# Kernel tuning notes

Hardware: AMD Instinct MI355X
Metric: run time of the kernel (lower is better)

The kernel has to match this reference:

```python
import jax, jax.numpy as jnp
import numpy as np

TEMPERATURE = 8.0  # sqrt(d_k=64)
NEG_FILL = -1000.0


def setup_inputs() -> dict:
    key = jax.random.key(0)
    k1, k2, k3, k4 = jax.random.split(key, 4)
    B, Lq, Lk, D = 16, 2048, 2048, 64
    q = jax.random.normal(k1, (B, Lq, D), dtype=jnp.float32)
    k = jax.random.normal(k2, (B, Lk, D), dtype=jnp.float32)
    v = jax.random.normal(k3, (B, Lk, D), dtype=jnp.float32)
    pad_mask = jax.random.randint(k4, (B, Lk), 0, 2).astype(bool)
    return {"q": q, "k": k, "v": v, "pad_mask": pad_mask}


def reference(q, k, v, pad_mask):
    # scores: [B, Lq, Lk]
    attn = jnp.einsum('bqd,bkd->bqk', q, k) / TEMPERATURE
    # mask padded keys (broadcast over query dim, like pad_mask.unsqueeze(1))
    attn = jnp.where(pad_mask[:, None, :], NEG_FILL, attn)
    attn = jax.nn.softmax(attn, axis=-1)
    # dropout is identity in eval / p=0
    output = jnp.einsum('bqk,bkd->bqd', attn, v)
    return output, attn
```

## Files before the change

kernel.cpp:

```cpp
#include <hip/hip_runtime.h>
#include <hip/hip_bf16.h>

#define BB 16
#define LL 2048
#define DD 64

typedef __attribute__((ext_vector_type(8))) short short8t;
typedef __attribute__((ext_vector_type(4))) float f32x4;
typedef __attribute__((ext_vector_type(4))) unsigned short ushort4t;

__device__ __forceinline__ unsigned short f2bf(float x) {
  union { float f; unsigned int u; } c; c.f = x;
  unsigned int u = c.u;
  u += 0x7fffu + ((u >> 16) & 1u);
  return (unsigned short)(u >> 16);
}

__global__ void cvt_bf16(const float* __restrict__ in, unsigned short* __restrict__ out) {
  int i = (blockIdx.x * 256 + threadIdx.x) * 4;
  float4 v = *(const float4*)(in + i);
  ushort4t o;
  o.x = f2bf(v.x); o.y = f2bf(v.y); o.z = f2bf(v.z); o.w = f2bf(v.w);
  *(ushort4t*)(out + i) = o;
}

__global__ void vtrans(const float* __restrict__ v, unsigned short* __restrict__ vt) {
  __shared__ unsigned short t[64][66];
  int b = blockIdx.x >> 5, j0 = (blockIdx.x & 31) * 64;
  const float* src = v + ((size_t)b * LL + j0) * DD;
#pragma unroll
  for (int i = 0; i < 16; ++i) {
    int lin = i * 256 + threadIdx.x;
    int j = lin >> 6, d = lin & 63;
    t[j][d] = f2bf(src[lin]);
  }
  __syncthreads();
  unsigned short* dst = vt + (size_t)b * DD * LL;
#pragma unroll
  for (int i = 0; i < 16; ++i) {
    int lin = i * 256 + threadIdx.x;
    int d = lin >> 6, j = lin & 63;
    dst[(size_t)d * LL + j0 + j] = t[j][d];
  }
}

__device__ __forceinline__ void async_cp16(const unsigned short* src, unsigned short* dst_lds) {
  __builtin_amdgcn_global_load_lds(
      (const __attribute__((address_space(1))) unsigned int*)src,
      (__attribute__((address_space(3))) unsigned int*)dst_lds, 16, 0, 0);
}

__global__ void __launch_bounds__(256, 2)
attn_main(const unsigned short* __restrict__ Qb, const unsigned short* __restrict__ Kb,
          const unsigned short* __restrict__ VTb, const int* __restrict__ mask,
          float* __restrict__ out, float* __restrict__ attn) {
  __shared__ __align__(16) unsigned short TB[4][3][2048];
  __shared__ float redL[4][64];
  __shared__ float rinvL[64];

  const int tid = threadIdx.x;
  const int w = tid >> 6;
  const int l = tid & 63;
  const int l15 = l & 15;
  const int g = l >> 4;

  const int b = blockIdx.x >> 5;
  const int q0 = (blockIdx.x & 31) << 6;

  unsigned short* KB = &TB[w][0][0];
  unsigned short* VB = &TB[w][1][0];
  unsigned short* PB = &TB[w][2][0];

  const unsigned short* Kbb = Kb + (size_t)b * LL * DD;
  const unsigned short* VTbb = VTb + (size_t)b * DD * LL;
  const int* maskb = mask + b * LL;

  short8t qf[4][2];
  {
    const unsigned short* qbase = Qb + ((size_t)b * LL + q0 + l15) * DD + 8 * g;
#pragma unroll
    for (int mi = 0; mi < 4; ++mi)
#pragma unroll
      for (int h = 0; h < 2; ++h)
        qf[mi][h] = *(const short8t*)(qbase + mi * 16 * DD + 32 * h);
  }

  float ls[4][4];
#pragma unroll
  for (int mi = 0; mi < 4; ++mi)
#pragma unroll
    for (int r = 0; r < 4; ++r) ls[mi][r] = 0.f;

  for (int t = w; t < 64; t += 4) {
    const int k0 = t * 32;
    {
      const unsigned short* gs = Kbb + (size_t)k0 * DD;
#pragma unroll
      for (int i = 0; i < 4; ++i) {
        int row = i * 8 + (l >> 3);
        int ce = (l & 7) * 8;
        async_cp16(gs + row * 64 + (ce ^ ((row & 3) << 4)), KB + i * 512);
      }
    }
    int mk0 = maskb[k0 + l15];
    int mk1 = maskb[k0 + 16 + l15];
    asm volatile("s_waitcnt vmcnt(0)" ::: "memory");

    f32x4 sacc[4][2] = {};
    short8t kf[2][2];
#pragma unroll
    for (int ni = 0; ni < 2; ++ni)
#pragma unroll
      for (int h = 0; h < 2; ++h) {
        int row = 16 * ni + l15;
        int col = (32 * h + 8 * g) ^ ((l15 & 3) << 4);
        kf[ni][h] = *(const short8t*)(KB + row * 64 + col);
      }
#pragma unroll
    for (int mi = 0; mi < 4; ++mi)
#pragma unroll
      for (int ni = 0; ni < 2; ++ni)
#pragma unroll
        for (int h = 0; h < 2; ++h)
          sacc[mi][ni] = __builtin_amdgcn_mfma_f32_16x16x32_bf16(qf[mi][h], kf[ni][h], sacc[mi][ni], 0, 0, 0);

#pragma unroll
    for (int mi = 0; mi < 4; ++mi)
#pragma unroll
      for (int ni = 0; ni < 2; ++ni) {
        int mk = ni ? mk1 : mk0;
#pragma unroll
        for (int r = 0; r < 4; ++r) {
          float sv = mk ? -1000.f : sacc[mi][ni][r] * 0.125f;
          ls[mi][r] += __expf(sv);
        }
      }
  }

#pragma unroll
  for (int mi = 0; mi < 4; ++mi)
#pragma unroll
    for (int r = 0; r < 4; ++r) {
      float s = ls[mi][r];
      s += __shfl_xor(s, 1);
      s += __shfl_xor(s, 2);
      s += __shfl_xor(s, 4);
      s += __shfl_xor(s, 8);
      if (l15 == 0) redL[w][16 * mi + 4 * g + r] = s;
    }
  __syncthreads();
  if (tid < 64)
    rinvL[tid] = 1.0f / (redL[0][tid] + redL[1][tid] + redL[2][tid] + redL[3][tid]);
  __syncthreads();

  float rinv_[4][4];
#pragma unroll
  for (int mi = 0; mi < 4; ++mi)
#pragma unroll
    for (int r = 0; r < 4; ++r) rinv_[mi][r] = rinvL[16 * mi + 4 * g + r];

  f32x4 oacc[4][4] = {};
  for (int t = w; t < 64; t += 4) {
    const int k0 = t * 32;
    {
      const unsigned short* gs = Kbb + (size_t)k0 * DD;
#pragma unroll
      for (int i = 0; i < 4; ++i) {
        int row = i * 8 + (l >> 3);
        int ce = (l & 7) * 8;
        async_cp16(gs + row * 64 + (ce ^ ((row & 3) << 4)), KB + i * 512);
      }
    }
    {
      const unsigned short* gs = VTbb + k0;
#pragma unroll
      for (int i = 0; i < 4; ++i) {
        int row = i * 16 + (l >> 2);
        int ce = (l & 3) * 8;
        async_cp16(gs + (size_t)row * LL + (ce ^ ((row & 1) << 4)), VB + i * 512);
      }
    }
    int mk0 = maskb[k0 + l15];
    int mk1 = maskb[k0 + 16 + l15];
    asm volatile("s_waitcnt vmcnt(0)" ::: "memory");

    f32x4 sacc[4][2] = {};
    short8t kf[2][2];
#pragma unroll
    for (int ni = 0; ni < 2; ++ni)
#pragma unroll
      for (int h = 0; h < 2; ++h) {
        int row = 16 * ni + l15;
        int col = (32 * h + 8 * g) ^ ((l15 & 3) << 4);
        kf[ni][h] = *(const short8t*)(KB + row * 64 + col);
      }
#pragma unroll
    for (int mi = 0; mi < 4; ++mi)
#pragma unroll
      for (int ni = 0; ni < 2; ++ni)
#pragma unroll
        for (int h = 0; h < 2; ++h)
          sacc[mi][ni] = __builtin_amdgcn_mfma_f32_16x16x32_bf16(qf[mi][h], kf[ni][h], sacc[mi][ni], 0, 0, 0);

#pragma unroll
    for (int mi = 0; mi < 4; ++mi)
#pragma unroll
      for (int ni = 0; ni < 2; ++ni) {
        int mk = ni ? mk1 : mk0;
#pragma unroll
        for (int r = 0; r < 4; ++r) {
          float sv = mk ? -1000.f : sacc[mi][ni][r] * 0.125f;
          float p = __expf(sv) * rinv_[mi][r];
          int qloc = 16 * mi + 4 * g + r;
          attn[((size_t)(b * LL + q0 + qloc)) * LL + k0 + 16 * ni + l15] = p;
          PB[qloc * 32 + ((16 * ni + l15) ^ ((r & 1) << 4))] = f2bf(p);
        }
      }

    short8t pf[4], vf[4];
#pragma unroll
    for (int mi = 0; mi < 4; ++mi)
      pf[mi] = *(const short8t*)(PB + (16 * mi + l15) * 32 + ((8 * g) ^ ((l & 1) << 4)));
#pragma unroll
    for (int ni = 0; ni < 4; ++ni)
      vf[ni] = *(const short8t*)(VB + (16 * ni + l15) * 32 + ((8 * g) ^ ((l & 1) << 4)));
#pragma unroll
    for (int mi = 0; mi < 4; ++mi)
#pragma unroll
      for (int ni = 0; ni < 4; ++ni)
        oacc[mi][ni] = __builtin_amdgcn_mfma_f32_16x16x32_bf16(pf[mi], vf[ni], oacc[mi][ni], 0, 0, 0);
  }

  __syncthreads();
  float* OB = (float*)&TB[0][0][0];
  if (w) {
#pragma unroll
    for (int mi = 0; mi < 4; ++mi)
#pragma unroll
      for (int ni = 0; ni < 4; ++ni)
#pragma unroll
        for (int r = 0; r < 4; ++r)
          OB[(w - 1) * 4096 + (16 * mi + 4 * g + r) * 64 + 16 * ni + l15] = oacc[mi][ni][r];
  }
  __syncthreads();
  if (w == 0) {
#pragma unroll
    for (int mi = 0; mi < 4; ++mi)
#pragma unroll
      for (int ni = 0; ni < 4; ++ni)
#pragma unroll
        for (int r = 0; r < 4; ++r) {
          int pos = (16 * mi + 4 * g + r) * 64 + 16 * ni + l15;
          float o = oacc[mi][ni][r] + OB[pos] + OB[4096 + pos] + OB[8192 + pos];
          out[((size_t)(b * LL + q0 + 16 * mi + 4 * g + r)) * DD + 16 * ni + l15] = o;
        }
  }
}

extern "C" void kernel_launch(void* const* d_in, const int* in_sizes, int n_in,
                              void* d_out, int out_size, void* d_ws, size_t ws_size,
                              hipStream_t stream) {
  const float* q = (const float*)d_in[0];
  const float* k = (const float*)d_in[1];
  const float* v = (const float*)d_in[2];
  const int* pm = (const int*)d_in[3];

  float* out = (float*)d_out;
  float* attn = out + (size_t)BB * LL * DD;

  unsigned short* Qb = (unsigned short*)d_ws;
  unsigned short* Kb = Qb + (size_t)BB * LL * DD;
  unsigned short* VT = Kb + (size_t)BB * LL * DD;

  cvt_bf16<<<2048, 256, 0, stream>>>(q, Qb);
  cvt_bf16<<<2048, 256, 0, stream>>>(k, Kb);
  vtrans<<<512, 256, 0, stream>>>(v, VT);
  attn_main<<<512, 256, 0, stream>>>(Qb, Kb, VT, pm, out, attn);
}
```

Baseline: 100.3 us.

## Repartition attention by query rows per wave with shared double-buffered K/V tiles

Merges the three preprocessing kernels into one prep launch. In the main kernel, each wave now owns 16 query rows and loops over all keys, instead of splitting the key range across waves. This removes the cross-wave softmax-sum and output reductions through LDS. K tiles of 128 keys are shared block-wide and double-buffered with async LDS loads; the next tile's K, V and mask are prefetched while MFMAs run. Probabilities are staged in LDS so attn is written with coalesced vector stores. Also adds block-index swizzling, setprio around MFMAs and masked-exp skipping, at the cost of more block barriers and more LDS per block.

New measurement: 103.9 us. 3.7% more time.

```diff
diff --git a/kernel.cpp b/kernel.cpp
--- a/kernel.cpp
+++ b/kernel.cpp
@@ -16,31 +16,38 @@
   return (unsigned short)(u >> 16);
 }
 
-__global__ void cvt_bf16(const float* __restrict__ in, unsigned short* __restrict__ out) {
-  int i = (blockIdx.x * 256 + threadIdx.x) * 4;
-  float4 v = *(const float4*)(in + i);
-  ushort4t o;
-  o.x = f2bf(v.x); o.y = f2bf(v.y); o.z = f2bf(v.z); o.w = f2bf(v.w);
-  *(ushort4t*)(out + i) = o;
-}
-
-__global__ void vtrans(const float* __restrict__ v, unsigned short* __restrict__ vt) {
+__global__ void prep(const float* __restrict__ q, const float* __restrict__ k,
+                     const float* __restrict__ v,
+                     unsigned short* __restrict__ Qb, unsigned short* __restrict__ Kb,
+                     unsigned short* __restrict__ VT) {
   __shared__ unsigned short t[64][66];
-  int b = blockIdx.x >> 5, j0 = (blockIdx.x & 31) * 64;
-  const float* src = v + ((size_t)b * LL + j0) * DD;
-#pragma unroll
-  for (int i = 0; i < 16; ++i) {
-    int lin = i * 256 + threadIdx.x;
-    int j = lin >> 6, d = lin & 63;
-    t[j][d] = f2bf(src[lin]);
-  }
-  __syncthreads();
-  unsigned short* dst = vt + (size_t)b * DD * LL;
-#pragma unroll
-  for (int i = 0; i < 16; ++i) {
-    int lin = i * 256 + threadIdx.x;
-    int d = lin >> 6, j = lin & 63;
-    dst[(size_t)d * LL + j0 + j] = t[j][d];
+  int bid = blockIdx.x;
+  if (bid < 4096) {
+    const float* in = (bid < 2048) ? q : k;
+    unsigned short* outp = (bid < 2048) ? Qb : Kb;
+    int i = (bid & 2047) * 1024 + threadIdx.x * 4;
+    float4 v4 = *(const float4*)(in + i);
+    ushort4t o;
+    o.x = f2bf(v4.x); o.y = f2bf(v4.y); o.z = f2bf(v4.z); o.w = f2bf(v4.w);
+    *(ushort4t*)(outp + i) = o;
+  } else {
+    int vb = bid - 4096;
+    int b = vb >> 5, j0 = (vb & 31) * 64;
+    const float* src = v + ((size_t)b * LL + j0) * DD;
+#pragma unroll
+    for (int i = 0; i < 16; ++i) {
+      int lin = i * 256 + threadIdx.x;
+      int j = lin >> 6, d = lin & 63;
+      t[j][d] = f2bf(src[lin]);
+    }
+    __syncthreads();
+    unsigned short* dst = VT + (size_t)b * DD * LL;
+#pragma unroll
+    for (int i = 0; i < 16; ++i) {
+      int lin = i * 256 + threadIdx.x;
+      int d = lin >> 6, j = lin & 63;
+      dst[(size_t)d * LL + j0 + j] = t[j][d];
+    }
   }
 }
 
@@ -54,9 +61,7 @@
 attn_main(const unsigned short* __restrict__ Qb, const unsigned short* __restrict__ Kb,
           const unsigned short* __restrict__ VTb, const int* __restrict__ mask,
           float* __restrict__ out, float* __restrict__ attn) {
-  __shared__ __align__(16) unsigned short TB[4][3][2048];
-  __shared__ float redL[4][64];
-  __shared__ float rinvL[64];
+  __shared__ __align__(16) unsigned short TB[40960];
 
   const int tid = threadIdx.x;
   const int w = tid >> 6;
@@ -64,197 +69,199 @@
   const int l15 = l & 15;
   const int g = l >> 4;
 
-  const int b = blockIdx.x >> 5;
-  const int q0 = (blockIdx.x & 31) << 6;
-
-  unsigned short* KB = &TB[w][0][0];
-  unsigned short* VB = &TB[w][1][0];
-  unsigned short* PB = &TB[w][2][0];
+  const int swzb = (blockIdx.x & 7) * 64 + (blockIdx.x >> 3);
+  const int b = swzb >> 5;
+  const int q0 = (swzb & 31) << 6;
+
+  unsigned short* KT0 = TB;
+  unsigned short* KT1 = TB + 8192;
+  unsigned short* VTt = TB + 16384;
+  float* PFw = (float*)(TB + 24576) + w * 2048;
 
   const unsigned short* Kbb = Kb + (size_t)b * LL * DD;
   const unsigned short* VTbb = VTb + (size_t)b * DD * LL;
   const int* maskb = mask + b * LL;
 
-  short8t qf[4][2];
+  auto stageK = [&](int t, unsigned short* KB) {
+    int k0 = (t & 15) * 128;
+    const unsigned short* gs = Kbb + (size_t)k0 * DD;
+#pragma unroll
+    for (int i2 = 0; i2 < 4; ++i2) {
+      int row = i2 * 32 + w * 8 + (l >> 3);
+      int ce = ((l & 7) * 8) ^ ((row & 3) << 4);
+      async_cp16(gs + row * 64 + ce, KB + (i2 * 32 + w * 8) * 64);
+    }
+  };
+  auto stageV = [&](int t) {
+    int k0 = (t & 15) * 128;
+#pragma unroll
+    for (int i2 = 0; i2 < 4; ++i2) {
+      int row = i2 * 16 + w * 4 + (l >> 4);
+      int ce = ((l & 15) * 8) ^ ((row & 3) << 4);
+      async_cp16(VTbb + (size_t)row * LL + k0 + ce, VTt + (i2 * 16 + w * 4) * 128);
+    }
+  };
+  auto loadMask = [&](int t, int* mk) {
+    int k0 = (t & 15) * 128;
+#pragma unroll
+    for (int ni = 0; ni < 8; ++ni) mk[ni] = maskb[k0 + 16 * ni + l15];
+  };
+
+  short8t qf[2];
   {
-    const unsigned short* qbase = Qb + ((size_t)b * LL + q0 + l15) * DD + 8 * g;
-#pragma unroll
-    for (int mi = 0; mi < 4; ++mi)
-#pragma unroll
-      for (int h = 0; h < 2; ++h)
-        qf[mi][h] = *(const short8t*)(qbase + mi * 16 * DD + 32 * h);
-  }
-
-  float ls[4][4];
-#pragma unroll
-  for (int mi = 0; mi < 4; ++mi)
-#pragma unroll
-    for (int r = 0; r < 4; ++r) ls[mi][r] = 0.f;
-
-  for (int t = w; t < 64; t += 4) {
-    const int k0 = t * 32;
-    {
-      const unsigned short* gs = Kbb + (size_t)k0 * DD;
-#pragma unroll
-      for (int i = 0; i < 4; ++i) {
-        int row = i * 8 + (l >> 3);
-        int ce = (l & 7) * 8;
-        async_cp16(gs + row * 64 + (ce ^ ((row & 3) << 4)), KB + i * 512);
+    const unsigned short* qbase = Qb + ((size_t)b * LL + q0 + 16 * w + l15) * DD + 8 * g;
+    qf[0] = *(const short8t*)(qbase);
+    qf[1] = *(const short8t*)(qbase + 32);
+  }
+
+  float ls[4] = {0.f, 0.f, 0.f, 0.f};
+  int mkA[8], mkB[8];
+
+  auto stepA = [&](int t, const unsigned short* KBc, unsigned short* KBn,
+                   const int* mkc, int* mkn) {
+    asm volatile("s_waitcnt vmcnt(0)" ::: "memory");
+    __syncthreads();
+    loadMask(t + 1, mkn);
+    stageK(t + 1, KBn);
+    __builtin_amdgcn_sched_barrier(0);
+    short8t kf[8][2];
+#pragma unroll
+    for (int ni = 0; ni < 8; ++ni)
+#pragma unroll
+      for (int h = 0; h < 2; ++h)
+        kf[ni][h] = *(const short8t*)(KBc + (16 * ni + l15) * 64 + ((32 * h + 8 * g) ^ ((l15 & 3) << 4)));
+    f32x4 sacc[8] = {};
+    __builtin_amdgcn_s_setprio(1);
+#pragma unroll
+    for (int ni = 0; ni < 8; ++ni)
+#pragma unroll
+      for (int h = 0; h < 2; ++h)
+        sacc[ni] = __builtin_amdgcn_mfma_f32_16x16x32_bf16(qf[h], kf[ni][h], sacc[ni], 0, 0, 0);
+    __builtin_amdgcn_s_setprio(0);
+#pragma unroll
+    for (int ni = 0; ni < 8; ++ni) {
+      int mk = mkc[ni];
+#pragma unroll
+      for (int r = 0; r < 4; ++r)
+        ls[r] += mk ? 0.f : __expf(sacc[ni][r] * 0.125f);
+    }
+  };
+
+  stageK(0, KT0);
+  loadMask(0, mkA);
+  for (int jj = 0; jj < 8; ++jj) {
+    stepA(2 * jj, KT0, KT1, mkA, mkB);
+    stepA(2 * jj + 1, KT1, KT0, mkB, mkA);
+  }
+
+  float rinv_[4];
+#pragma unroll
+  for (int r = 0; r < 4; ++r) {
+    float s = ls[r];
+    s += __shfl_xor(s, 1);
+    s += __shfl_xor(s, 2);
+    s += __shfl_xor(s, 4);
+    s += __shfl_xor(s, 8);
+    rinv_[r] = 1.0f / s;
+  }
+
+  f32x4 oacc[4] = {};
+  const size_t abase0 = (size_t)(b * LL + q0 + 16 * w) * LL;
+
+  auto stepB = [&](int t, bool first, const unsigned short* KBc, unsigned short* KBn,
+                   const int* mkc, int* mkn) {
+    if (first) { asm volatile("s_waitcnt vmcnt(0)" ::: "memory"); }
+    else       { asm volatile("s_waitcnt vmcnt(8)" ::: "memory"); }
+    __syncthreads();
+    const int k0 = (t & 15) * 128;
+
+    short8t vf[4][4];
+#pragma unroll
+    for (int kk = 0; kk < 4; ++kk)
+#pragma unroll
+      for (int ni = 0; ni < 4; ++ni)
+        vf[kk][ni] = *(const short8t*)(VTt + (16 * ni + l15) * 128 + ((32 * kk + 8 * g) ^ ((l15 & 3) << 4)));
+    asm volatile("s_waitcnt lgkmcnt(0)" ::: "memory");
+    __builtin_amdgcn_sched_barrier(0);
+    __syncthreads();
+
+    loadMask(t + 1, mkn);
+    stageK(t + 1, KBn);
+    stageV(t + 1);
+    __builtin_amdgcn_sched_barrier(0);
+
+    short8t kf[8][2];
+#pragma unroll
+    for (int ni = 0; ni < 8; ++ni)
+#pragma unroll
+      for (int h = 0; h < 2; ++h)
+        kf[ni][h] = *(const short8t*)(KBc + (16 * ni + l15) * 64 + ((32 * h + 8 * g) ^ ((l15 & 3) << 4)));
+    f32x4 sacc[8] = {};
+    __builtin_amdgcn_s_setprio(1);
+#pragma unroll
+    for (int ni = 0; ni < 8; ++ni)
+#pragma unroll
+      for (int h = 0; h < 2; ++h)
+        sacc[ni] = __builtin_amdgcn_mfma_f32_16x16x32_bf16(qf[h], kf[ni][h], sacc[ni], 0, 0, 0);
+    __builtin_amdgcn_s_setprio(0);
+
+#pragma unroll
+    for (int ni = 0; ni < 8; ++ni) {
+      int mk = mkc[ni];
+#pragma unroll
+      for (int r = 0; r < 4; ++r) {
+        float p = mk ? 0.f : __expf(sacc[ni][r] * 0.125f) * rinv_[r];
+        PFw[(4 * g + r) * 128 + ((16 * ni + l15) ^ ((g & 1) << 4))] = p;
       }
     }
-    int mk0 = maskb[k0 + l15];
-    int mk1 = maskb[k0 + 16 + l15];
-    asm volatile("s_waitcnt vmcnt(0)" ::: "memory");
-
-    f32x4 sacc[4][2] = {};
-    short8t kf[2][2];
-#pragma unroll
-    for (int ni = 0; ni < 2; ++ni)
-#pragma unroll
-      for (int h = 0; h < 2; ++h) {
-        int row = 16 * ni + l15;
-        int col = (32 * h + 8 * g) ^ ((l15 & 3) << 4);
-        kf[ni][h] = *(const short8t*)(KB + row * 64 + col);
-      }
-#pragma unroll
-    for (int mi = 0; mi < 4; ++mi)
-#pragma unroll
-      for (int ni = 0; ni < 2; ++ni)
-#pragma unroll
-        for (int h = 0; h < 2; ++h)
-          sacc[mi][ni] = __builtin_amdgcn_mfma_f32_16x16x32_bf16(qf[mi][h], kf[ni][h], sacc[mi][ni], 0, 0, 0);
-
-#pragma unroll
-    for (int mi = 0; mi < 4; ++mi)
-#pragma unroll
-      for (int ni = 0; ni < 2; ++ni) {
-        int mk = ni ? mk1 : mk0;
-#pragma unroll
-        for (int r = 0; r < 4; ++r) {
-          float sv = mk ? -1000.f : sacc[mi][ni][r] * 0.125f;
-          ls[mi][r] += __expf(sv);
-        }
-      }
-  }
-
-#pragma unroll
-  for (int mi = 0; mi < 4; ++mi)
-#pragma unroll
-    for (int r = 0; r < 4; ++r) {
-      float s = ls[mi][r];
-      s += __shfl_xor(s, 1);
-      s += __shfl_xor(s, 2);
-      s += __shfl_xor(s, 4);
-      s += __shfl_xor(s, 8);
-      if (l15 == 0) redL[w][16 * mi + 4 * g + r] = s;
-    }
-  __syncthreads();
-  if (tid < 64)
-    rinvL[tid] = 1.0f / (redL[0][tid] + redL[1][tid] + redL[2][tid] + redL[3][tid]);
-  __syncthreads();
-
-  float rinv_[4][4];
-#pragma unroll
-  for (int mi = 0; mi < 4; ++mi)
-#pragma unroll
-    for (int r = 0; r < 4; ++r) rinv_[mi][r] = rinvL[16 * mi + 4 * g + r];
-
-  f32x4 oacc[4][4] = {};
-  for (int t = w; t < 64; t += 4) {
-    const int k0 = t * 32;
-    {
-      const unsigned short* gs = Kbb + (size_t)k0 * DD;
-#pragma unroll
-      for (int i = 0; i < 4; ++i) {
-        int row = i * 8 + (l >> 3);
-        int ce = (l & 7) * 8;
-        async_cp16(gs + row * 64 + (ce ^ ((row & 3) << 4)), KB + i * 512);
-      }
-    }
-    {
-      const unsigned short* gs = VTbb + k0;
-#pragma unroll
-      for (int i = 0; i < 4; ++i) {
-        int row = i * 16 + (l >> 2);
-        int ce = (l & 3) * 8;
-        async_cp16(gs + (size_t)row * LL + (ce ^ ((row & 1) << 4)), VB + i * 512);
-      }
-    }
-    int mk0 = maskb[k0 + l15];
-    int mk1 = maskb[k0 + 16 + l15];
-    asm volatile("s_waitcnt vmcnt(0)" ::: "memory");
-
-    f32x4 sacc[4][2] = {};
-    short8t kf[2][2];
-#pragma unroll
-    for (int ni = 0; ni < 2; ++ni)
-#pragma unroll
-      for (int h = 0; h < 2; ++h) {
-        int row = 16 * ni + l15;
-        int col = (32 * h + 8 * g) ^ ((l15 & 3) << 4);
-        kf[ni][h] = *(const short8t*)(KB + row * 64 + col);
-      }
-#pragma unroll
-    for (int mi = 0; mi < 4; ++mi)
-#pragma unroll
-      for (int ni = 0; ni < 2; ++ni)
-#pragma unroll
-        for (int h = 0; h < 2; ++h)
-          sacc[mi][ni] = __builtin_amdgcn_mfma_f32_16x16x32_bf16(qf[mi][h], kf[ni][h], sacc[mi][ni], 0, 0, 0);
-
-#pragma unroll
-    for (int mi = 0; mi < 4; ++mi)
-#pragma unroll
-      for (int ni = 0; ni < 2; ++ni) {
-        int mk = ni ? mk1 : mk0;
-#pragma unroll
-        for (int r = 0; r < 4; ++r) {
-          float sv = mk ? -1000.f : sacc[mi][ni][r] * 0.125f;
-          float p = __expf(sv) * rinv_[mi][r];
-          int qloc = 16 * mi + 4 * g + r;
-          attn[((size_t)(b * LL + q0 + qloc)) * LL + k0 + 16 * ni + l15] = p;
-          PB[qloc * 32 + ((16 * ni + l15) ^ ((r & 1) << 4))] = f2bf(p);
-        }
-      }
-
-    short8t pf[4], vf[4];
-#pragma unroll
-    for (int mi = 0; mi < 4; ++mi)
-      pf[mi] = *(const short8t*)(PB + (16 * mi + l15) * 32 + ((8 * g) ^ ((l & 1) << 4)));
-#pragma unroll
-    for (int ni = 0; ni < 4; ++ni)
-      vf[ni] = *(const short8t*)(VB + (16 * ni + l15) * 32 + ((8 * g) ^ ((l & 1) << 4)));
-#pragma unroll
-    for (int mi = 0; mi < 4; ++mi)
+    asm volatile("s_waitcnt lgkmcnt(0)" ::: "memory");
+    __builtin_amdgcn_sched_barrier(0);
+
+#pragma unroll
+    for (int it = 0; it < 8; ++it) {
+      int row = l >> 2;
+      int cb = (l & 3) * 4 + 16 * it;
+      f32x4 pv = *(const f32x4*)(PFw + row * 128 + (cb ^ (((row >> 2) & 1) << 4)));
+      *(f32x4*)(attn + abase0 + (size_t)row * LL + k0 + cb) = pv;
+    }
+
+    short8t pfr[4];
+#pragma unroll
+    for (int kk = 0; kk < 4; ++kk) {
+      const float* src = PFw + l15 * 128 + ((32 * kk + 8 * g) ^ (((l15 >> 2) & 1) << 4));
+      f32x4 pa = *(const f32x4*)(src);
+      f32x4 pb = *(const f32x4*)(src + 4);
+      short8t f;
+      f[0] = (short)f2bf(pa[0]); f[1] = (short)f2bf(pa[1]);
+      f[2] = (short)f2bf(pa[2]); f[3] = (short)f2bf(pa[3]);
+      f[4] = (short)f2bf(pb[0]); f[5] = (short)f2bf(pb[1]);
+      f[6] = (short)f2bf(pb[2]); f[7] = (short)f2bf(pb[3]);
+      pfr[kk] = f;
+    }
+    __builtin_amdgcn_s_setprio(1);
+#pragma unroll
+    for (int kk = 0; kk < 4; ++kk)
 #pragma unroll
       for (int ni = 0; ni < 4; ++ni)
-        oacc[mi][ni] = __builtin_amdgcn_mfma_f32_16x16x32_bf16(pf[mi], vf[ni], oacc[mi][ni], 0, 0, 0);
-  }
-
-  __syncthreads();
-  float* OB = (float*)&TB[0][0][0];
-  if (w) {
-#pragma unroll
-    for (int mi = 0; mi < 4; ++mi)
-#pragma unroll
-      for (int ni = 0; ni < 4; ++ni)
-#pragma unroll
-        for (int r = 0; r < 4; ++r)
-          OB[(w - 1) * 4096 + (16 * mi + 4 * g + r) * 64 + 16 * ni + l15] = oacc[mi][ni][r];
-  }
-  __syncthreads();
-  if (w == 0) {
-#pragma unroll
-    for (int mi = 0; mi < 4; ++mi)
-#pragma unroll
-      for (int ni = 0; ni < 4; ++ni)
-#pragma unroll
-        for (int r = 0; r < 4; ++r) {
-          int pos = (16 * mi + 4 * g + r) * 64 + 16 * ni + l15;
-          float o = oacc[mi][ni][r] + OB[pos] + OB[4096 + pos] + OB[8192 + pos];
-          out[((size_t)(b * LL + q0 + 16 * mi + 4 * g + r)) * DD + 16 * ni + l15] = o;
-        }
-  }
+        oacc[ni] = __builtin_amdgcn_mfma_f32_16x16x32_bf16(pfr[kk], vf[kk][ni], oacc[ni], 0, 0, 0);
+    __builtin_amdgcn_s_setprio(0);
+  };
+
+  stageV(0);
+  stepB(0, true, KT0, KT1, mkA, mkB);
+  for (int jj = 0; jj < 7; ++jj) {
+    stepB(2 * jj + 1, false, KT1, KT0, mkB, mkA);
+    stepB(2 * jj + 2, false, KT0, KT1, mkA, mkB);
+  }
+  stepB(15, false, KT1, KT0, mkB, mkA);
+
+  asm volatile("s_waitcnt vmcnt(0)" ::: "memory");
+
+#pragma unroll
+  for (int ni = 0; ni < 4; ++ni)
+#pragma unroll
+    for (int r = 0; r < 4; ++r)
+      out[(size_t)(b * LL + q0 + 16 * w + 4 * g + r) * DD + 16 * ni + l15] = oacc[ni][r];
 }
 
 extern "C" void kernel_launch(void* const* d_in, const int* in_sizes, int n_in,
@@ -272,8 +279,6 @@
   unsigned short* Kb = Qb + (size_t)BB * LL * DD;
   unsigned short* VT = Kb + (size_t)BB * LL * DD;
 
-  cvt_bf16<<<2048, 256, 0, stream>>>(q, Qb);
-  cvt_bf16<<<2048, 256, 0, stream>>>(k, Kb);
-  vtrans<<<512, 256, 0, stream>>>(v, VT);
+  prep<<<4608, 256, 0, stream>>>(q, k, v, Qb, Kb, VT);
   attn_main<<<512, 256, 0, stream>>>(Qb, Kb, VT, pm, out, attn);
 }
```
